# Kernel optimization log

Hardware: AMD Instinct MI355X
Metric: run time of the kernel (lower is better)

The kernel has to match this reference:

```python
import jax, jax.numpy as jnp
import numpy as np

D_K = 1024
NHEADS = 16
HEAD_DIM = D_K // NHEADS  # 64
STD = float(np.sqrt(HEAD_DIM))  # matches math.sqrt(d_k // nheads)


def setup_inputs() -> dict:
    key = jax.random.key(0)
    ks = jax.random.split(key, 9)
    B, S = 2, 2048
    scale = 1.0 / np.sqrt(D_K)
    x = jax.random.normal(ks[0], (B, S, D_K), dtype=jnp.float32)
    Wq = jax.random.normal(ks[1], (D_K, D_K), dtype=jnp.float32) * scale
    bq = jnp.zeros((D_K,), dtype=jnp.float32)
    Wk = jax.random.normal(ks[2], (D_K, D_K), dtype=jnp.float32) * scale
    bk = jnp.zeros((D_K,), dtype=jnp.float32)
    Wv = jax.random.normal(ks[3], (D_K, D_K), dtype=jnp.float32) * scale
    bv = jnp.zeros((D_K,), dtype=jnp.float32)
    Wo = jax.random.normal(ks[4], (D_K, D_K), dtype=jnp.float32) * scale
    bo = jnp.zeros((D_K,), dtype=jnp.float32)
    return {"x": x, "Wq": Wq, "bq": bq, "Wk": Wk, "bk": bk,
            "Wv": Wv, "bv": bv, "Wo": Wo, "bo": bo}


def _heads(x, W, b):
    # Linear then split heads: (B,S,D) -> (B,H,S,hd)
    B, S, _ = x.shape
    out = x @ W.T + b
    return out.reshape(B, S, NHEADS, HEAD_DIM).transpose(0, 2, 1, 3)


def reference(x, Wq, bq, Wk, bk, Wv, bv, Wo, bo):
    B, S, _ = x.shape
    q = _heads(x, Wq, bq)  # (B,H,S,hd)
    k = _heads(x, Wk, bk)
    v = _heads(x, Wv, bv)
    scores = jnp.einsum('bhqd,bhkd->bhqk', q, k) / STD  # (B,H,S,S)
    causal = jnp.tril(jnp.ones((S, S), dtype=bool))  # mask_factory default
    scores = jnp.where(causal[None, None, :, :], scores, -jnp.inf)
    attn = jax.nn.softmax(scores, axis=-1)
    ctx = jnp.einsum('bhqk,bhkd->bhqd', attn, v)  # (B,H,S,hd)
    ctx = ctx.transpose(0, 2, 1, 3).reshape(B, S, D_K)
    return ctx @ Wo.T + bo
```

## Files before the change

### kernel.cpp

```cpp
#include <hip/hip_runtime.h>
#include <stdint.h>

typedef unsigned short u16;
typedef __bf16 bf16x8 __attribute__((ext_vector_type(8)));
typedef __bf16 bf16x4v __attribute__((ext_vector_type(4)));
typedef float f32x4 __attribute__((ext_vector_type(4)));

typedef __attribute__((address_space(3))) uint32_t lds_u32;
typedef __attribute__((address_space(1))) uint32_t glb_u32;

__device__ __forceinline__ f32x4 mfma16(bf16x8 a, bf16x8 b, f32x4 c) {
    return __builtin_amdgcn_mfma_f32_16x16x32_bf16(a, b, c, 0, 0, 0);
}

__device__ __forceinline__ ushort4 pk4(float a, float b, float c, float d) {
    bf16x4v v;
    v[0] = (__bf16)a; v[1] = (__bf16)b; v[2] = (__bf16)c; v[3] = (__bf16)d;
    union { bf16x4v v; ushort4 u; } cv; cv.v = v; return cv.u;
}

__device__ __forceinline__ float fexp2(float x) {
    return __builtin_amdgcn_exp2f(x);
}

__device__ __forceinline__ void async16(const u16* g, u16* l) {
    __builtin_amdgcn_global_load_lds((glb_u32*)(uintptr_t)(const void*)g,
                                     (lds_u32*)l, 16, 0, 0);
}

__global__ __launch_bounds__(256) void cast_all(
    const float* __restrict__ x,
    const float* __restrict__ w0, const float* __restrict__ w1,
    const float* __restrict__ w2, const float* __restrict__ w3,
    u16* __restrict__ xo, u16* __restrict__ o0, u16* __restrict__ o1,
    u16* __restrict__ o2, u16* __restrict__ o3)
{
    const int s = blockIdx.y;
    const int i = (blockIdx.x * 256 + threadIdx.x) * 4;
    if (s == 0) {
#pragma unroll
        for (int c = 0; c < 4; ++c) {
            const int j = i + c * (1 << 20);
            float4 v = *(const float4*)(x + j);
            *(ushort4*)(xo + j) = pk4(v.x, v.y, v.z, v.w);
        }
    } else {
        const float* in = s == 1 ? w0 : (s == 2 ? w1 : (s == 3 ? w2 : w3));
        u16* out       = s == 1 ? o0 : (s == 2 ? o1 : (s == 3 ? o2 : o3));
        float4 v = *(const float4*)(in + i);
        *(ushort4*)(out + i) = pk4(v.x, v.y, v.z, v.w);
    }
}

__global__ __launch_bounds__(256) void gemm_qkv(
    const u16* __restrict__ A,
    const u16* __restrict__ W0, const u16* __restrict__ W1, const u16* __restrict__ W2,
    const float* __restrict__ B0, const float* __restrict__ B1, const float* __restrict__ B2,
    u16* __restrict__ O0, u16* __restrict__ O1,
    u16* __restrict__ VT,
    int M, int N, int K)
{
    const int x = blockIdx.x & 7;
    const int L = blockIdx.x >> 3;
    const int tm = (8 * (x >> 1) + (L & 7)) << 7;
    const int tnsel = 12 * (x & 1) + (L >> 3);
    const int sel = tnsel >> 3;
    const int tn  = (tnsel & 7) << 7;

    const u16* W      = sel == 0 ? W0 : (sel == 1 ? W1 : W2);
    const float* bias = sel == 0 ? B0 : (sel == 1 ? B1 : B2);
    u16* O            = sel == 0 ? O0 : O1;

    __shared__ __attribute__((aligned(16))) u16 As[2][128 * 64];
    __shared__ __attribute__((aligned(16))) u16 Bs[2][128 * 64];
    u16 (*Tb)[136] = (u16 (*)[136])As;

    const int tid  = threadIdx.x;
    const int lane = tid & 63;
    const int w    = tid >> 6;
    const int l15  = lane & 15;
    const int quad = lane >> 4;

    const int wm = (w >> 1) << 6;
    const int wn = (w & 1) << 6;

    f32x4 acc[4][4];
#pragma unroll
    for (int i = 0; i < 4; ++i)
#pragma unroll
        for (int j = 0; j < 4; ++j) acc[i][j] = f32x4{0.f, 0.f, 0.f, 0.f};

    const int lr  = lane >> 3;
    const int lcc = lane & 7;
    const int scc = lcc ^ lr;
    const u16* Ag = A + (size_t)(tm + 32 * w + lr) * K + scc * 8;
    const u16* Wg = W + (size_t)(tn + 32 * w + lr) * K + scc * 8;
    u16* Al = &As[0][(32 * w + lr) * 64 + lcc * 8];
    u16* Bl = &Bs[0][(32 * w + lr) * 64 + lcc * 8];

#define QKV_STAGE(bi, k0)                                                      \
    do {                                                                       \
        _Pragma("unroll")                                                      \
        for (int m = 0; m < 4; ++m) {                                          \
            async16(Ag + (k0) + (size_t)m * 8 * K, Al + (bi) * 8192 + m * 512);\
            async16(Wg + (k0) + (size_t)m * 8 * K, Bl + (bi) * 8192 + m * 512);\
        }                                                                      \
    } while (0)

    const int nt = K >> 6;
    QKV_STAGE(0, 0);
    for (int t = 0; t < nt; ++t) {
        const int cur = t & 1;
        asm volatile("s_waitcnt vmcnt(0)" ::: "memory");
        __syncthreads();
        if (t + 1 < nt) QKV_STAGE(cur ^ 1, (t + 1) * 64);
        const u16* Ab = As[cur];
        const u16* Bb = Bs[cur];
#pragma unroll
        for (int kk = 0; kk < 2; ++kk) {
            bf16x8 a[4], b[4];
#pragma unroll
            for (int i = 0; i < 4; ++i) {
                const int r  = wm + 16 * i + l15;
                const int sl = (kk * 4 + quad) ^ (r & 7);
                a[i] = *(const bf16x8*)&Ab[r * 64 + sl * 8];
            }
#pragma unroll
            for (int j = 0; j < 4; ++j) {
                const int r  = wn + 16 * j + l15;
                const int sl = (kk * 4 + quad) ^ (r & 7);
                b[j] = *(const bf16x8*)&Bb[r * 64 + sl * 8];
            }
#pragma unroll
            for (int i = 0; i < 4; ++i)
#pragma unroll
                for (int j = 0; j < 4; ++j)
                    acc[i][j] = mfma16(a[i], b[j], acc[i][j]);
        }
    }
#undef QKV_STAGE

    if (sel == 2) {
        const int bb = tm >> 11;
        const int s0 = tm & 2047;
        const size_t vtb = ((size_t)bb << 10) + tn;
        for (int c32 = 0; c32 < 128; c32 += 32) {
            __syncthreads();
            if ((c32 >> 6) == (wn >> 6)) {
                const int j0 = (c32 >> 4) & 2;
#pragma unroll
                for (int jj = 0; jj < 2; ++jj) {
                    const int j  = j0 + jj;
                    const int cc = jj * 16 + l15;
                    const float bj = bias[tn + wn + 16 * j + l15];
#pragma unroll
                    for (int i = 0; i < 4; ++i) {
                        const int rr = wm + 16 * i + quad * 4;
                        *(ushort4*)&Tb[cc][rr] =
                            pk4(acc[i][j][0] + bj, acc[i][j][1] + bj,
                                acc[i][j][2] + bj, acc[i][j][3] + bj);
                    }
                }
            }
            __syncthreads();
            {
                const int c  = tid >> 3;
                const int ss = (tid & 7) * 16;
                uint4 v0 = *(const uint4*)&Tb[c][ss];
                uint4 v1 = *(const uint4*)&Tb[c][ss + 8];
                u16* dst = &VT[(vtb + c32 + c) * 2048 + s0 + ss];
                *(uint4*)dst       = v0;
                *(uint4*)(dst + 8) = v1;
            }
        }
    } else {
#pragma unroll
        for (int j = 0; j < 4; ++j) {
            const int col = tn + wn + 16 * j + l15;
            const float bj = bias[col];
#pragma unroll
            for (int i = 0; i < 4; ++i) {
                const int row = tm + wm + 16 * i + quad * 4;
#pragma unroll
                for (int r = 0; r < 4; ++r) {
                    union { float f; unsigned u; } v; v.f = acc[i][j][r] + bj;
                    unsigned rn = v.u + 0x7FFFu + ((v.u >> 16) & 1u);
                    O[(size_t)(row + r) * N + col] = (u16)(rn >> 16);
                }
            }
        }
    }
}

__global__ __launch_bounds__(256) void gemm_out64(
    const u16* __restrict__ A, const u16* __restrict__ W,
    const float* __restrict__ bias, float* __restrict__ O,
    int M, int N, int K)
{
    __shared__ __attribute__((aligned(16))) u16 As[2][128 * 64];
    __shared__ __attribute__((aligned(16))) u16 Bs[2][64 * 64];

    const int x = blockIdx.x & 7;
    const int L = blockIdx.x >> 3;
    const int tm = (8 * (x >> 1) + (L & 7)) << 7;
    const int tn = (8 * (x & 1) + (L >> 3)) << 6;

    const int tid  = threadIdx.x;
    const int lane = tid & 63;
    const int w    = tid >> 6;
    const int l15  = lane & 15;
    const int quad = lane >> 4;

    const int wm = (w >> 1) << 6;
    const int wn = (w & 1) << 5;

    f32x4 acc[4][2];
#pragma unroll
    for (int i = 0; i < 4; ++i)
#pragma unroll
        for (int j = 0; j < 2; ++j) acc[i][j] = f32x4{0.f, 0.f, 0.f, 0.f};

    const int lr  = lane >> 3;
    const int lcc = lane & 7;
    const int scc = lcc ^ lr;
    const u16* Ag = A + (size_t)(tm + 32 * w + lr) * K + scc * 8;
    const u16* Wg = W + (size_t)(tn + 16 * w + lr) * K + scc * 8;
    u16* Al = &As[0][(32 * w + lr) * 64 + lcc * 8];
    u16* Bl = &Bs[0][(16 * w + lr) * 64 + lcc * 8];

#define OUT_STAGE(bi, k0)                                                      \
    do {                                                                       \
        _Pragma("unroll")                                                      \
        for (int m = 0; m < 4; ++m)                                            \
            async16(Ag + (k0) + (size_t)m * 8 * K, Al + (bi) * 8192 + m * 512);\
        _Pragma("unroll")                                                      \
        for (int m = 0; m < 2; ++m)                                            \
            async16(Wg + (k0) + (size_t)m * 8 * K, Bl + (bi) * 4096 + m * 512);\
    } while (0)

    const int nt = K >> 6;
    OUT_STAGE(0, 0);
    for (int t = 0; t < nt; ++t) {
        const int cur = t & 1;
        asm volatile("s_waitcnt vmcnt(0)" ::: "memory");
        __syncthreads();
        if (t + 1 < nt) OUT_STAGE(cur ^ 1, (t + 1) * 64);
        const u16* Ab = As[cur];
        const u16* Bb = Bs[cur];
#pragma unroll
        for (int kk = 0; kk < 2; ++kk) {
            bf16x8 a[4], b[2];
#pragma unroll
            for (int i = 0; i < 4; ++i) {
                const int r  = wm + 16 * i + l15;
                const int sl = (kk * 4 + quad) ^ (r & 7);
                a[i] = *(const bf16x8*)&Ab[r * 64 + sl * 8];
            }
#pragma unroll
            for (int j = 0; j < 2; ++j) {
                const int r  = wn + 16 * j + l15;
                const int sl = (kk * 4 + quad) ^ (r & 7);
                b[j] = *(const bf16x8*)&Bb[r * 64 + sl * 8];
            }
#pragma unroll
            for (int i = 0; i < 4; ++i)
#pragma unroll
                for (int j = 0; j < 2; ++j)
                    acc[i][j] = mfma16(a[i], b[j], acc[i][j]);
        }
    }
#undef OUT_STAGE

#pragma unroll
    for (int j = 0; j < 2; ++j) {
        const int col = tn + wn + 16 * j + l15;
        const float bj = bias[col];
#pragma unroll
        for (int i = 0; i < 4; ++i) {
            const int row = tm + wm + 16 * i + quad * 4;
#pragma unroll
            for (int r = 0; r < 4; ++r)
                O[(size_t)(row + r) * N + col] = acc[i][j][r] + bj;
        }
    }
}

__device__ __forceinline__ bf16x8 rdt(const u16* base, int t, int l15, int cc) {
    const int r = t * 16 + l15;
    const int c = (cc & 3) ^ ((r >> 1) & 3);
    return *(const bf16x8*)(base + (cc >> 2) * 2048 + r * 32 + c * 8);
}

#define QK_EXP(Z, PROW, QG, MASKED, RSV, KB)                                   \
    do {                                                                       \
        _Pragma("unroll")                                                      \
        for (int t = 0; t < 4; ++t) {                                          \
            float e0 = fexp2(fmaf((Z)[t][0], SC, -16.0f));                     \
            float e1 = fexp2(fmaf((Z)[t][1], SC, -16.0f));                     \
            float e2 = fexp2(fmaf((Z)[t][2], SC, -16.0f));                     \
            float e3 = fexp2(fmaf((Z)[t][3], SC, -16.0f));                     \
            if (MASKED) {                                                      \
                const int kb = (KB) + t * 16 + quad * 4;                       \
                if (kb + 0 > (QG)) e0 = 0.f;                                   \
                if (kb + 1 > (QG)) e1 = 0.f;                                   \
                if (kb + 2 > (QG)) e2 = 0.f;                                   \
                if (kb + 3 > (QG)) e3 = 0.f;                                   \
            }                                                                  \
            (RSV)[0] += e0; (RSV)[1] += e1;                                    \
            (RSV)[2] += e2; (RSV)[3] += e3;                                    \
            *(ushort4*)((PROW) + (((2 * t + whi) ^ sl7) << 3) + woff) =        \
                pk4(e0, e1, e2, e3);                                           \
        }                                                                      \
    } while (0)

__global__ __launch_bounds__(256, 4) void attn11(
    const u16* __restrict__ Q, const u16* __restrict__ Kb,
    const u16* __restrict__ VT, u16* __restrict__ ctx)
{
    __shared__ __attribute__((aligned(16))) u16 Kt[2][4096];
    __shared__ __attribute__((aligned(16))) u16 Vt[2][4096];
    __shared__ __attribute__((aligned(16))) u16 Pt[4][16][64];

    const int tid  = threadIdx.x;
    const int lane = tid & 63;
    const int wid  = tid >> 6;
    const int l15  = lane & 15;
    const int quad = lane >> 4;
    const int sl7  = l15 & 7;
    const int whi  = quad >> 1;
    const int woff = (quad & 1) * 4;

    const int hb = blockIdx.x & 31;
    const int h  = hb & 15, b = hb >> 4;
    const int ti = blockIdx.x >> 5;
    const int tq = ti >> 3, to = ti & 7;
    const int g4 = (tq == 0) ? to
                 : (tq == 1) ? (15 - to)
                 : (tq == 2) ? (16 + to)
                 :             (31 - to);
    const int s  = 4 * g4 + wid;
    const int NT = g4 + 1;

    const size_t rowbase = (size_t)b * 2048;
    const int cbase = h * 64;
    const u16* kbase = Kb + rowbase * 1024 + cbase;
    const u16* vbase = VT + ((size_t)b * 1024 + cbase) * 2048;

    const int qg = s * 16 + l15;
    const u16* qp = Q + (rowbase + qg) * 1024 + cbase + quad * 8;
    const bf16x8 q0 = *(const bf16x8*)qp, q1 = *(const bf16x8*)(qp + 32);

    const int sr  = tid >> 2;
    const int sc0 = (((tid & 3) ^ ((sr >> 1) & 3)) << 3);
    const u16* kg = kbase + (size_t)sr * 1024 + sc0;
    const u16* vg = vbase + (size_t)sr * 2048 + sc0;

    f32x4 o[4];
#pragma unroll
    for (int i = 0; i < 4; ++i) o[i] = f32x4{0, 0, 0, 0};
    f32x4 rsv = {0, 0, 0, 0};
    const float SC = 0.18033688011112042f;

    u16 (*ptw)[64] = Pt[wid];
    u16* const pr = &ptw[l15][0];
    const int pof0 = (quad ^ sl7) << 3;
    const int pof1 = ((quad | 4) ^ sl7) << 3;

#define STAGE(buf, Tt)                                                         \
    do {                                                                       \
        const u16* kq = kg + (size_t)(Tt) * 65536;                             \
        const u16* vq = vg + (Tt) * 64;                                        \
        async16(kq,      &Kt[buf][tid * 8]);                                   \
        async16(kq + 32, &Kt[buf][2048 + tid * 8]);                            \
        async16(vq,      &Vt[buf][tid * 8]);                                   \
        async16(vq + 32, &Vt[buf][2048 + tid * 8]);                            \
    } while (0)

    STAGE(0, 0);

    for (int T = 0; T < NT; ++T) {
        const int cur = T & 1;
        asm volatile("s_waitcnt vmcnt(0)" ::: "memory");
        __syncthreads();
        if (T + 1 < NT) STAGE(cur ^ 1, T + 1);

        const u16* KT = Kt[cur];
        const u16* VL = Vt[cur];

        f32x4 z[4];
        __builtin_amdgcn_s_setprio(1);
#pragma unroll
        for (int t = 0; t < 4; ++t) {
            const bf16x8 kA = rdt(KT, t, l15, quad);
            const bf16x8 kB = rdt(KT, t, l15, quad + 4);
            f32x4 zz = {0, 0, 0, 0};
            zz = mfma16(kA, q0, zz);
            zz = mfma16(kB, q1, zz);
            z[t] = zz;
        }
        __builtin_amdgcn_s_setprio(0);

        if (T == NT - 1) QK_EXP(z, pr, qg, 1, rsv, T * 64);
        else             QK_EXP(z, pr, qg, 0, rsv, T * 64);

        const bf16x8 pb0 = *(const bf16x8*)(pr + pof0);
        const bf16x8 pb1 = *(const bf16x8*)(pr + pof1);

        __builtin_amdgcn_s_setprio(1);
#pragma unroll
        for (int t = 0; t < 4; ++t) {
            const bf16x8 vA = rdt(VL, t, l15, quad);
            const bf16x8 vB = rdt(VL, t, l15, quad + 4);
            o[t] = mfma16(vA, pb0, o[t]);
            o[t] = mfma16(vB, pb1, o[t]);
        }
        __builtin_amdgcn_s_setprio(0);
    }
#undef STAGE

    float rs = (rsv[0] + rsv[1]) + (rsv[2] + rsv[3]);
    rs += __shfl_xor(rs, 16); rs += __shfl_xor(rs, 32);
    const float inv = 1.0f / rs;
#pragma unroll
    for (int t = 0; t < 4; ++t) {
        *(ushort4*)&ctx[(rowbase + qg) * 1024 + cbase + t * 16 + quad * 4] =
            pk4(o[t][0] * inv, o[t][1] * inv, o[t][2] * inv, o[t][3] * inv);
    }
}

extern "C" void kernel_launch(void* const* d_in, const int* in_sizes, int n_in,
                              void* d_out, int out_size, void* d_ws, size_t ws_size,
                              hipStream_t stream) {
    const float* x  = (const float*)d_in[0];
    const float* Wq = (const float*)d_in[1];
    const float* bq = (const float*)d_in[2];
    const float* Wk = (const float*)d_in[3];
    const float* bk = (const float*)d_in[4];
    const float* Wv = (const float*)d_in[5];
    const float* bv = (const float*)d_in[6];
    const float* Wo = (const float*)d_in[7];
    const float* bo = (const float*)d_in[8];
    float* out = (float*)d_out;

    const int N = 1024, K = 1024;
    const int M = in_sizes[0] / K;
    const size_t MN = (size_t)M * N;
    const size_t WN = (size_t)N * K;

    u16* xb  = (u16*)d_ws;
    u16* wqb = xb  + MN;
    u16* wkb = wqb + WN;
    u16* wvb = wkb + WN;
    u16* wob = wvb + WN;
    u16* q   = wob + WN;
    u16* kb  = q   + MN;
    u16* vt  = kb  + MN;
    u16* ctx = q;

    cast_all<<<dim3(1024, 5), 256, 0, stream>>>(
        x, Wq, Wk, Wv, Wo, xb, wqb, wkb, wvb, wob);

    gemm_qkv<<<dim3(768), 256, 0, stream>>>(
        xb, wqb, wkb, wvb, bq, bk, bv, q, kb, vt, M, N, K);

    attn11<<<dim3(1024), 256, 0, stream>>>(q, kb, vt, ctx);

    gemm_out64<<<dim3(512), 256, 0, stream>>>(
        ctx, wob, bo, out, M, N, K);
}
```

Measured before the change: 178.2 us.

## Permute K tile rows so softmax probabilities feed PV MFMA from registers

The K tile is now loaded into shared memory with a permuted row order. This makes the QK^T MFMA output layout match the B-operand layout the PV MFMA expects, so the exponentiated probabilities can be packed straight into registers. The per-wave P scratch buffer in shared memory, its swizzled stores and reloads, and the implicit wave-level dependency go away. The causal mask index is recomputed to follow the permuted key order. Correctness depends on the bit permutation matching exactly across the MFMA layouts.

Result: no change. 177.7 us (-0.2%).

```diff
diff --git a/kernel.cpp b/kernel.cpp
--- a/kernel.cpp
+++ b/kernel.cpp
@@ -291,44 +291,18 @@
     return *(const bf16x8*)(base + (cc >> 2) * 2048 + r * 32 + c * 8);
 }
 
-#define QK_EXP(Z, PROW, QG, MASKED, RSV, KB)                                   \
-    do {                                                                       \
-        _Pragma("unroll")                                                      \
-        for (int t = 0; t < 4; ++t) {                                          \
-            float e0 = fexp2(fmaf((Z)[t][0], SC, -16.0f));                     \
-            float e1 = fexp2(fmaf((Z)[t][1], SC, -16.0f));                     \
-            float e2 = fexp2(fmaf((Z)[t][2], SC, -16.0f));                     \
-            float e3 = fexp2(fmaf((Z)[t][3], SC, -16.0f));                     \
-            if (MASKED) {                                                      \
-                const int kb = (KB) + t * 16 + quad * 4;                       \
-                if (kb + 0 > (QG)) e0 = 0.f;                                   \
-                if (kb + 1 > (QG)) e1 = 0.f;                                   \
-                if (kb + 2 > (QG)) e2 = 0.f;                                   \
-                if (kb + 3 > (QG)) e3 = 0.f;                                   \
-            }                                                                  \
-            (RSV)[0] += e0; (RSV)[1] += e1;                                    \
-            (RSV)[2] += e2; (RSV)[3] += e3;                                    \
-            *(ushort4*)((PROW) + (((2 * t + whi) ^ sl7) << 3) + woff) =        \
-                pk4(e0, e1, e2, e3);                                           \
-        }                                                                      \
-    } while (0)
-
-__global__ __launch_bounds__(256, 4) void attn11(
+__global__ __launch_bounds__(256, 4) void attn12(
     const u16* __restrict__ Q, const u16* __restrict__ Kb,
     const u16* __restrict__ VT, u16* __restrict__ ctx)
 {
     __shared__ __attribute__((aligned(16))) u16 Kt[2][4096];
     __shared__ __attribute__((aligned(16))) u16 Vt[2][4096];
-    __shared__ __attribute__((aligned(16))) u16 Pt[4][16][64];
 
     const int tid  = threadIdx.x;
     const int lane = tid & 63;
     const int wid  = tid >> 6;
     const int l15  = lane & 15;
     const int quad = lane >> 4;
-    const int sl7  = l15 & 7;
-    const int whi  = quad >> 1;
-    const int woff = (quad & 1) * 4;
 
     const int hb = blockIdx.x & 31;
     const int h  = hb & 15, b = hb >> 4;
@@ -351,8 +325,9 @@
     const bf16x8 q0 = *(const bf16x8*)qp, q1 = *(const bf16x8*)(qp + 32);
 
     const int sr  = tid >> 2;
+    const int psr = (sr & 0x23) | ((sr & 0x0C) << 1) | ((sr & 0x10) >> 2);
     const int sc0 = (((tid & 3) ^ ((sr >> 1) & 3)) << 3);
-    const u16* kg = kbase + (size_t)sr * 1024 + sc0;
+    const u16* kg = kbase + (size_t)psr * 1024 + sc0;
     const u16* vg = vbase + (size_t)sr * 2048 + sc0;
 
     f32x4 o[4];
@@ -360,11 +335,6 @@
     for (int i = 0; i < 4; ++i) o[i] = f32x4{0, 0, 0, 0};
     f32x4 rsv = {0, 0, 0, 0};
     const float SC = 0.18033688011112042f;
-
-    u16 (*ptw)[64] = Pt[wid];
-    u16* const pr = &ptw[l15][0];
-    const int pof0 = (quad ^ sl7) << 3;
-    const int pof1 = ((quad | 4) ^ sl7) << 3;
 
 #define STAGE(buf, Tt)                                                         \
     do {                                                                       \
@@ -400,11 +370,36 @@
         }
         __builtin_amdgcn_s_setprio(0);
 
-        if (T == NT - 1) QK_EXP(z, pr, qg, 1, rsv, T * 64);
-        else             QK_EXP(z, pr, qg, 0, rsv, T * 64);
-
-        const bf16x8 pb0 = *(const bf16x8*)(pr + pof0);
-        const bf16x8 pb1 = *(const bf16x8*)(pr + pof1);
+        float e[4][4];
+        if (T == NT - 1) {
+#pragma unroll
+            for (int t = 0; t < 4; ++t)
+#pragma unroll
+                for (int r = 0; r < 4; ++r) {
+                    const int kreal = T * 64 + ((t & 2) << 4) + (quad << 3)
+                                    + ((t & 1) << 2) + r;
+                    float v = fmaf(z[t][r], SC, -16.0f);
+                    const float ev = fexp2(v);
+                    e[t][r] = (kreal > qg) ? 0.f : ev;
+                    rsv[r] += e[t][r];
+                }
+        } else {
+#pragma unroll
+            for (int t = 0; t < 4; ++t)
+#pragma unroll
+                for (int r = 0; r < 4; ++r) {
+                    e[t][r] = fexp2(fmaf(z[t][r], SC, -16.0f));
+                    rsv[r] += e[t][r];
+                }
+        }
+
+        union { ushort4 q[2]; bf16x8 v; } cv0, cv1;
+        cv0.q[0] = pk4(e[0][0], e[0][1], e[0][2], e[0][3]);
+        cv0.q[1] = pk4(e[1][0], e[1][1], e[1][2], e[1][3]);
+        cv1.q[0] = pk4(e[2][0], e[2][1], e[2][2], e[2][3]);
+        cv1.q[1] = pk4(e[3][0], e[3][1], e[3][2], e[3][3]);
+        const bf16x8 pb0 = cv0.v;
+        const bf16x8 pb1 = cv1.v;
 
         __builtin_amdgcn_s_setprio(1);
 #pragma unroll
@@ -463,7 +458,7 @@
     gemm_qkv<<<dim3(768), 256, 0, stream>>>(
         xb, wqb, wkb, wvb, bq, bk, bv, q, kb, vt, M, N, K);
 
-    attn11<<<dim3(1024), 256, 0, stream>>>(q, kb, vt, ctx);
+    attn12<<<dim3(1024), 256, 0, stream>>>(q, kb, vt, ctx);
 
     gemm_out64<<<dim3(512), 256, 0, stream>>>(
         ctx, wob, bo, out, M, N, K);
```
